# Kernel tuning notes

Hardware: AMD Instinct MI355X
Metric: run time of the kernel (lower is better)

Reference implementation:

```python
import jax, jax.numpy as jnp
import numpy as np

BIT_W = 8   # config.bit_wt
BIT_A = 8   # config.bit_act (activations sliced 2 bits at a time)
STRIDE = (1, 1)
PAD = 1


def _conv(a, w):
    # NCHW input, OIHW weight, stride 1, symmetric padding 1 (matches wrapped Conv2d)
    return jax.lax.conv_general_dilated(
        a, w, window_strides=STRIDE, padding=[(PAD, PAD), (PAD, PAD)],
        dimension_numbers=("NCHW", "OIHW", "NCHW"))


def setup_inputs() -> dict:
    key = jax.random.key(0)
    k1, k2, k3 = jax.random.split(key, 3)
    x = jax.random.normal(k1, (64, 64, 56, 56), dtype=jnp.float32)
    weight = jax.random.normal(k2, (64, 64, 3, 3), dtype=jnp.float32)
    bias = jax.random.normal(k3, (64,), dtype=jnp.float32)
    scale_a = jnp.full((1,), 20.0, dtype=jnp.float32)      # conv_q.scale
    scale_w = jnp.full((1,), 20.0, dtype=jnp.float32)      # wrapped_module.weight_scale
    zero_point = jnp.full((1,), -128.0, dtype=jnp.float32)  # conv_q.zero_point
    return {"x": x, "weight": weight, "bias": bias,
            "scale_a": scale_a, "scale_w": scale_w, "zero_point": zero_point}


def reference(x, weight, bias, scale_a, scale_w, zero_point):
    sa = scale_a[0]
    sw = scale_w[0]
    zp = zero_point[0]
    # activation quantization: round(x*scale_a - zero_point), clamp to [0, 2^bit_act - 1]
    q_in = jnp.clip(jnp.round(x * sa - zp), 0.0, 2.0 ** BIT_A - 1.0)
    # weight quantization: round(w * scale_w), interpreted in two's complement
    q_w = jnp.round(weight * sw)
    w_off = q_w + 2.0 ** BIT_W  # (w + (1 << bit_weight)) before bit masking

    acc = jnp.zeros((), dtype=jnp.float32)
    for ba in range(BIT_A // 2):
        # 2-bit activation slice: (a >> 2*ba) & 3
        a_sl = jnp.mod(jnp.floor(q_in / (4.0 ** ba)), 4.0)
        for bw in range(BIT_W):
            # weight bit bw: ((w + 2^B) >> bw) & 1
            w_bit = jnp.mod(jnp.floor(w_off / (2.0 ** bw)), 2.0)
            r = _conv(a_sl, w_bit)
            sgn = -1.0 if bw == BIT_W - 1 else 1.0  # MSB = sign bit (two's complement)
            acc = acc + sgn * (2.0 ** (2 * ba + bw)) * r

    # zero-point correction: conv(ones * zp, q_w) added back (no-op when zp == 0)
    acc = acc + zp * _conv(jnp.ones_like(q_in), q_w)

    out = acc / (sw * sa) + bias[None, :, None, None]
    return out
```

## Files before the change

### kernel.cpp

```cpp
#include <hip/hip_runtime.h>


typedef int v4i __attribute__((ext_vector_type(4)));

#define QA_ROW   3712
#define QA_IMG   215296
#define QA_BYTES 13778944

__global__ __launch_bounds__(64) void prep_wq(const float* __restrict__ wt,
                                              const float* __restrict__ sw_p,
                                              const float* __restrict__ zp_p,
                                              signed char* __restrict__ w8,
                                              float* __restrict__ corr_tab) {
  const int o = blockIdx.x;
  const int i = threadIdx.x;
  const float sw = sw_p[0];
  const float* wp = wt + (size_t)(o * 64 + i) * 9;
  int q[9];
#pragma unroll
  for (int k = 0; k < 9; ++k) q[k] = (int)rintf(wp[k] * sw);
#pragma unroll
  for (int k = 0; k < 9; ++k)
    w8[(o * 9 + k) * 64 + i] = (signed char)(q[k] & 255);

  int stc[9], srw[9];
#pragma unroll
  for (int k = 0; k < 9; ++k) {
    int a = (int)(signed char)(q[k] & 255);
    int b = q[k];
#pragma unroll
    for (int off = 32; off; off >>= 1) {
      a += __shfl_xor(a, off);
      b += __shfl_xor(b, off);
    }
    stc[k] = a; srw[k] = b;
  }
  const float zp = zp_p[0];
  if (i < 9) {
    const int v = i / 3, hc = i % 3;
    float corr = 0.0f;
#pragma unroll
    for (int k = 0; k < 9; ++k) {
      const int kh = k / 3, kw = k % 3;
      const bool drop = (v == 1 && kh == 0) || (v == 2 && kh == 2) ||
                        (hc == 1 && kw == 0) || (hc == 2 && kw == 2);
      if (!drop) corr += 128.0f * (float)stc[k] + zp * (float)srw[k];
    }
    corr_tab[i * 64 + o] = corr;
  }
}

__global__ __launch_bounds__(256) void quant_a(const float* __restrict__ x,
                                               const float* __restrict__ sa_p,
                                               const float* __restrict__ zp_p,
                                               signed char* __restrict__ qa) {
  __shared__ int ldsbuf[1904];
  signed char* lds = (signed char*)ldsbuf;
  const int bx = blockIdx.x;
  const int n = blockIdx.y;
  const int t = threadIdx.x;
  const float sa = sa_p[0], zp = zp_p[0];
  const float* xim = x + (size_t)n * 200704;
  const int h0 = bx * 2;

#pragma unroll
  for (int it = 0; it < 7; ++it) {
    const int idx = t + 256 * it;
    const int r = idx >= 896;
    const int rem = idx - 896 * r;
    const int c = (rem * 2341) >> 15;
    const int w4 = rem - c * 14;
    const float4 v = *(const float4*)(xim + (size_t)c * 3136 + (h0 + r) * 56 + w4 * 4);
    signed char* dst = lds + r * 3808 + w4 * 272 + c;
    const float vv[4] = {v.x, v.y, v.z, v.w};
#pragma unroll
    for (int e = 0; e < 4; ++e) {
      float tq;
      {
#pragma clang fp contract(off)
        tq = vv[e] * sa - zp;
      }
      float qf = rintf(tq);
      qf = fminf(fmaxf(qf, 0.0f), 255.0f);
      dst[e * 68] = (signed char)((int)qf - 128);
    }
  }
  __syncthreads();

  signed char* const qim = qa + (size_t)n * QA_IMG;
#pragma unroll
  for (int it = 0; it < 2; ++it) {
    const int idx = t + 256 * it;
    if (idx < 448) {
      const int r = idx >= 224;
      const int u = idx - 224 * r;
      const int w = u >> 2, q2 = u & 3;
      const unsigned* s = (const unsigned*)(lds + r * 3808 + w * 68 + q2 * 16);
      const uint4 vv = make_uint4(s[0], s[1], s[2], s[3]);
      *((uint4*)(qim + (size_t)(h0 + r + 1) * QA_ROW + (w + 1) * 64 + q2 * 16)) = vv;
    } else if (idx < 464) {
      const int p = idx - 448;
      const int r = p >> 3;
      const int side = (p >> 2) & 1;
      const int j = p & 3;
      *((uint4*)(qim + (size_t)(h0 + r + 1) * QA_ROW + side * 57 * 64 + j * 16)) =
          make_uint4(0, 0, 0, 0);
    }
  }
  if (bx == 0 && t < 232)
    ((uint4*)qim)[t] = make_uint4(0, 0, 0, 0);
  if (bx == 27 && t < 232)
    ((uint4*)(qim + (size_t)57 * QA_ROW))[t] = make_uint4(0, 0, 0, 0);
}

__global__ __launch_bounds__(256, 4) void conv_mfma(
    const signed char* __restrict__ qa, const signed char* __restrict__ w8,
    const float* __restrict__ corr_tab, const float* __restrict__ bias,
    const float* __restrict__ sa_p, const float* __restrict__ sw_p,
    float* __restrict__ out) {
  __shared__ __align__(16) signed char lds[24576];
  const int tid = threadIdx.x;
  const int n = blockIdx.y;
  const int h0 = blockIdx.x * 4;

  {
    const uint4* src = (const uint4*)(qa + (size_t)n * QA_IMG + (size_t)h0 * QA_ROW);
    const uint4* csrc = (const uint4*)corr_tab;
    uint4* dst = (uint4*)lds;
#pragma unroll
    for (int it = 0; it < 6; ++it) {
      const int idx = tid + it * 256;
      uint4 v;
      if (idx < 1392) v = src[idx];
      else v = csrc[idx - 1392];
      dst[idx] = v;
    }
  }
  __syncthreads();

  const int lane = tid & 63;
  const int wv = tid >> 6;
  const int phalf = wv & 1;
  const int ogp = wv >> 1;
  const int ln = lane & 15;
  const int kg = lane >> 4;
  const int oa = ogp * 32 + ln;

  const signed char* wba = w8 + (size_t)oa * 576 + kg * 16;
  v4i Ba[9], Bb[9];
#pragma unroll
  for (int t = 0; t < 9; ++t) {
    Ba[t] = *(const v4i*)(wba + t * 64);
    Bb[t] = *(const v4i*)(wba + 9216 + t * 64);
  }

  const float sa = sa_p[0], sw = sw_p[0];
  const float rden = 1.0f / (sw * sa);
  const float boa = bias[oa], bob = bias[oa + 16];
  const float* ctab = (const float*)(lds + 22272);
  const float cFa = ctab[oa];
  const float cFb = ctab[oa + 16];
  float* const outa = out + (size_t)(n * 64 + oa) * 3136 + h0 * 56;
  float* const outb = outa + 16 * 3136;

#pragma unroll 1
  for (int t = 0; t < 7; ++t) {
    const int pb = phalf * 112 + t * 16;
    const int pa = pb + ln;
    const int hr = (pa * 9363) >> 19;
    const int wc = pa - hr * 56;
    const signed char* ab = lds + (hr * 58 + wc) * 64 + kg * 16;
    v4i acca = {0, 0, 0, 0}, accb = {0, 0, 0, 0};
#pragma unroll
    for (int kh = 0; kh < 3; ++kh) {
#pragma unroll
      for (int kw = 0; kw < 3; ++kw) {
        const v4i A = *(const v4i*)(ab + (kh * 58 + kw) * 64);
        acca = __builtin_amdgcn_mfma_i32_16x16x64_i8(A, Ba[kh * 3 + kw], acca, 0, 0, 0);
        accb = __builtin_amdgcn_mfma_i32_16x16x64_i8(A, Bb[kh * 3 + kw], accb, 0, 0, 0);
      }
    }
    const int pxb = pb + kg * 4;
    float ta[4], tb[4];
#pragma unroll
    for (int e = 0; e < 4; ++e) {
      const int p = pxb + e;
      const int hh = (p * 9363) >> 19;
      const int ww = p - hh * 56;
      const int hg = h0 + hh;
      float ca = cFa, cb = cFb;
      if ((hg == 0) | (hg == 55) | (ww == 0) | (ww == 55)) {
        const int vcase = (hg == 0) ? 1 : ((hg == 55) ? 2 : 0);
        const int hcase = (ww == 0) ? 1 : ((ww == 55) ? 2 : 0);
        const int cidx = (vcase * 3 + hcase) * 64;
        ca = ctab[cidx + oa];
        cb = ctab[cidx + oa + 16];
      }
      ta[e] = ((float)acca[e] + ca) * rden + boa;
      tb[e] = ((float)accb[e] + cb) * rden + bob;
    }
    *(float4*)(outa + pxb) = make_float4(ta[0], ta[1], ta[2], ta[3]);
    *(float4*)(outb + pxb) = make_float4(tb[0], tb[1], tb[2], tb[3]);
  }
}

extern "C" void kernel_launch(void* const* d_in, const int* in_sizes, int n_in,
                              void* d_out, int out_size, void* d_ws, size_t ws_size,
                              hipStream_t stream) {
  const float* x    = (const float*)d_in[0];
  const float* wt   = (const float*)d_in[1];
  const float* bias = (const float*)d_in[2];
  const float* sa   = (const float*)d_in[3];
  const float* sw   = (const float*)d_in[4];
  const float* zp   = (const float*)d_in[5];
  float* out = (float*)d_out;

  char* ws = (char*)d_ws;
  signed char* qa = (signed char*)ws;
  signed char* w8 = (signed char*)(ws + QA_BYTES);
  float* corr_tab = (float*)(ws + QA_BYTES + 36864);

  prep_wq<<<64, 64, 0, stream>>>(wt, sw, zp, w8, corr_tab);
  quant_a<<<dim3(28, 64), 256, 0, stream>>>(x, sa, zp, qa);
  conv_mfma<<<dim3(14, 64), 256, 0, stream>>>(qa, w8, corr_tab, bias, sa, sw, out);
}
```

Measured before the change: 126.0 us.

## Fuse activation quantization into the conv kernel, dropping the intermediate int8 buffer

Removes the separate quant_a kernel and its global int8 padded activation buffer. Each conv block now reads the six fp32 input rows it needs (four output rows plus halo), quantizes and transposes them through a staging area in shared memory, and writes the padded tile directly into LDS. This removes one launch and the global write and read of the quantized tensor. In exchange, halo rows are quantized twice by neighbouring blocks, LDS use per block rises, and the loads now occur in three serialized phases with barriers before the MFMA loop starts.

```diff
diff --git a/kernel.cpp b/kernel.cpp
--- a/kernel.cpp
+++ b/kernel.cpp
@@ -2,10 +2,6 @@
 
 
 typedef int v4i __attribute__((ext_vector_type(4)));
-
-#define QA_ROW   3712
-#define QA_IMG   215296
-#define QA_BYTES 13778944
 
 __global__ __launch_bounds__(64) void prep_wq(const float* __restrict__ wt,
                                               const float* __restrict__ sw_p,
@@ -50,93 +46,78 @@
   }
 }
 
-__global__ __launch_bounds__(256) void quant_a(const float* __restrict__ x,
-                                               const float* __restrict__ sa_p,
-                                               const float* __restrict__ zp_p,
-                                               signed char* __restrict__ qa) {
-  __shared__ int ldsbuf[1904];
-  signed char* lds = (signed char*)ldsbuf;
-  const int bx = blockIdx.x;
-  const int n = blockIdx.y;
-  const int t = threadIdx.x;
-  const float sa = sa_p[0], zp = zp_p[0];
-  const float* xim = x + (size_t)n * 200704;
-  const int h0 = bx * 2;
-
-#pragma unroll
-  for (int it = 0; it < 7; ++it) {
-    const int idx = t + 256 * it;
-    const int r = idx >= 896;
-    const int rem = idx - 896 * r;
-    const int c = (rem * 2341) >> 15;
-    const int w4 = rem - c * 14;
-    const float4 v = *(const float4*)(xim + (size_t)c * 3136 + (h0 + r) * 56 + w4 * 4);
-    signed char* dst = lds + r * 3808 + w4 * 272 + c;
-    const float vv[4] = {v.x, v.y, v.z, v.w};
-#pragma unroll
-    for (int e = 0; e < 4; ++e) {
-      float tq;
-      {
-#pragma clang fp contract(off)
-        tq = vv[e] * sa - zp;
-      }
-      float qf = rintf(tq);
-      qf = fminf(fmaxf(qf, 0.0f), 255.0f);
-      dst[e * 68] = (signed char)((int)qf - 128);
-    }
-  }
-  __syncthreads();
-
-  signed char* const qim = qa + (size_t)n * QA_IMG;
-#pragma unroll
-  for (int it = 0; it < 2; ++it) {
-    const int idx = t + 256 * it;
-    if (idx < 448) {
-      const int r = idx >= 224;
-      const int u = idx - 224 * r;
-      const int w = u >> 2, q2 = u & 3;
-      const unsigned* s = (const unsigned*)(lds + r * 3808 + w * 68 + q2 * 16);
-      const uint4 vv = make_uint4(s[0], s[1], s[2], s[3]);
-      *((uint4*)(qim + (size_t)(h0 + r + 1) * QA_ROW + (w + 1) * 64 + q2 * 16)) = vv;
-    } else if (idx < 464) {
-      const int p = idx - 448;
-      const int r = p >> 3;
-      const int side = (p >> 2) & 1;
-      const int j = p & 3;
-      *((uint4*)(qim + (size_t)(h0 + r + 1) * QA_ROW + side * 57 * 64 + j * 16)) =
-          make_uint4(0, 0, 0, 0);
-    }
-  }
-  if (bx == 0 && t < 232)
-    ((uint4*)qim)[t] = make_uint4(0, 0, 0, 0);
-  if (bx == 27 && t < 232)
-    ((uint4*)(qim + (size_t)57 * QA_ROW))[t] = make_uint4(0, 0, 0, 0);
-}
-
-__global__ __launch_bounds__(256, 4) void conv_mfma(
-    const signed char* __restrict__ qa, const signed char* __restrict__ w8,
+__global__ __launch_bounds__(256, 4) void conv_fused(
+    const float* __restrict__ x, const signed char* __restrict__ w8,
     const float* __restrict__ corr_tab, const float* __restrict__ bias,
     const float* __restrict__ sa_p, const float* __restrict__ sw_p,
-    float* __restrict__ out) {
-  __shared__ __align__(16) signed char lds[24576];
+    const float* __restrict__ zp_p, float* __restrict__ out) {
+  __shared__ __align__(16) signed char lds[32192];
+  signed char* const trbuf = lds + 24576;
+
   const int tid = threadIdx.x;
   const int n = blockIdx.y;
   const int h0 = blockIdx.x * 4;
-
-  {
-    const uint4* src = (const uint4*)(qa + (size_t)n * QA_IMG + (size_t)h0 * QA_ROW);
-    const uint4* csrc = (const uint4*)corr_tab;
-    uint4* dst = (uint4*)lds;
-#pragma unroll
-    for (int it = 0; it < 6; ++it) {
-      const int idx = tid + it * 256;
-      uint4 v;
-      if (idx < 1392) v = src[idx];
-      else v = csrc[idx - 1392];
-      dst[idx] = v;
-    }
-  }
-  __syncthreads();
+  const float sa = sa_p[0], zp = zp_p[0];
+  const float* xim = x + (size_t)n * 200704;
+
+#pragma unroll 1
+  for (int p = 0; p < 3; ++p) {
+    const int ihb = h0 - 1 + 2 * p;
+#pragma unroll
+    for (int it = 0; it < 7; ++it) {
+      const int idx = tid + 256 * it;
+      const int r = idx >= 896;
+      const int rem = idx - 896 * r;
+      const int c = (rem * 2341) >> 15;
+      const int w4 = rem - c * 14;
+      const int ih = ihb + r;
+      const bool valid = (unsigned)ih < 56u;
+      float4 v = make_float4(0.0f, 0.0f, 0.0f, 0.0f);
+      if (valid)
+        v = *(const float4*)(xim + (size_t)c * 3136 + ih * 56 + w4 * 4);
+      signed char* dst = trbuf + r * 3808 + w4 * 272 + c;
+      const float vv[4] = {v.x, v.y, v.z, v.w};
+#pragma unroll
+      for (int e = 0; e < 4; ++e) {
+        signed char b = 0;
+        if (valid) {
+          float tq;
+          {
+#pragma clang fp contract(off)
+            tq = vv[e] * sa - zp;
+          }
+          float qf = rintf(tq);
+          qf = fminf(fmaxf(qf, 0.0f), 255.0f);
+          b = (signed char)((int)qf - 128);
+        }
+        dst[e * 68] = b;
+      }
+    }
+    __syncthreads();
+    const int cnt = p ? 464 : 608;
+#pragma unroll
+    for (int it = 0; it < 3; ++it) {
+      const int idx = tid + 256 * it;
+      if (idx < 448) {
+        const int r = idx >= 224;
+        const int u = idx - 224 * r;
+        const int w = u >> 2, q2 = u & 3;
+        const unsigned* s = (const unsigned*)(trbuf + r * 3808 + w * 68 + q2 * 16);
+        const uint4 vv = make_uint4(s[0], s[1], s[2], s[3]);
+        *((uint4*)(lds + ((2 * p + r) * 58 + w + 1) * 64 + q2 * 16)) = vv;
+      } else if (idx < 464) {
+        const int p2 = idx - 448;
+        const int r = p2 >> 3;
+        const int side = (p2 >> 2) & 1;
+        const int j = p2 & 3;
+        *((uint4*)(lds + ((2 * p + r) * 58 + side * 57) * 64 + j * 16)) =
+            make_uint4(0, 0, 0, 0);
+      } else if (idx < cnt) {
+        ((uint4*)(lds + 22272))[idx - 464] = ((const uint4*)corr_tab)[idx - 464];
+      }
+    }
+    __syncthreads();
+  }
 
   const int lane = tid & 63;
   const int wv = tid >> 6;
@@ -154,7 +135,7 @@
     Bb[t] = *(const v4i*)(wba + 9216 + t * 64);
   }
 
-  const float sa = sa_p[0], sw = sw_p[0];
+  const float sw = sw_p[0];
   const float rden = 1.0f / (sw * sa);
   const float boa = bias[oa], bob = bias[oa + 16];
   const float* ctab = (const float*)(lds + 22272);
@@ -184,9 +165,9 @@
     float ta[4], tb[4];
 #pragma unroll
     for (int e = 0; e < 4; ++e) {
-      const int p = pxb + e;
-      const int hh = (p * 9363) >> 19;
-      const int ww = p - hh * 56;
+      const int px = pxb + e;
+      const int hh = (px * 9363) >> 19;
+      const int ww = px - hh * 56;
       const int hg = h0 + hh;
       float ca = cFa, cb = cFb;
       if ((hg == 0) | (hg == 55) | (ww == 0) | (ww == 55)) {
@@ -216,11 +197,9 @@
   float* out = (float*)d_out;
 
   char* ws = (char*)d_ws;
-  signed char* qa = (signed char*)ws;
-  signed char* w8 = (signed char*)(ws + QA_BYTES);
-  float* corr_tab = (float*)(ws + QA_BYTES + 36864);
+  signed char* w8 = (signed char*)ws;
+  float* corr_tab = (float*)(ws + 36864);
 
   prep_wq<<<64, 64, 0, stream>>>(wt, sw, zp, w8, corr_tab);
-  quant_a<<<dim3(28, 64), 256, 0, stream>>>(x, sa, zp, qa);
-  conv_mfma<<<dim3(14, 64), 256, 0, stream>>>(qa, w8, corr_tab, bias, sa, sw, out);
+  conv_fused<<<dim3(14, 64), 256, 0, stream>>>(x, w8, corr_tab, bias, sa, sw, zp, out);
 }
```

Measured after the change: 128.4 us. About the same (+2.0%).
